# Kernel tuning notes

Hardware: AMD Instinct MI355X
Metric: run time of the kernel (lower is better)

Reference implementation:

```python
import jax, jax.numpy as jnp
import numpy as np

MEAN_DEG = 3.8
QS = (2, 4, 8, 16, 32, 64)
POOL_DIM = 100
BP_ITERS = 10


def _bn(x, g, b):
    # BatchNorm1d in training mode: biased batch statistics over the node dim
    m = x.mean(0)
    v = ((x - m) ** 2).mean(0)
    return g * (x - m) * jax.lax.rsqrt(v + 1e-5) + b


def _gcn_sparse(x, src, dst, n, w, b):
    # GCNConv: add self loops, symmetric deg^-1/2 normalization, scatter-add aggregation
    loop = jnp.arange(n, dtype=src.dtype)
    s2 = jnp.concatenate([src, loop])
    d2 = jnp.concatenate([dst, loop])
    deg = jax.ops.segment_sum(jnp.ones(s2.shape[0], x.dtype), d2, num_segments=n)
    dinv = jnp.where(deg > 0, jax.lax.rsqrt(deg), 0.0)
    norm = (dinv[s2] * dinv[d2])[:, None]
    return jax.ops.segment_sum((x @ w)[s2] * norm, d2, num_segments=n) + b


def _gcn_dense(x, adj, w, b):
    # GCN on the dense pooled adjacency (pooled graphs are fully connected)
    n = adj.shape[-1]
    A = adj + jnp.eye(n, dtype=adj.dtype)
    d = A.sum(-1)
    dinv = jnp.where(d > 0, jax.lax.rsqrt(d), 0.0)
    An = dinv[:, :, None] * A * dinv[:, None, :]
    return jnp.einsum('bij,bjd->bid', An, x @ w) + b


def _bp(src, dst, n, q, beta, seed):
    # SBM-style belief propagation: iterate node marginals psi [n,q] for a fixed
    # number of sweeps; coupling exp(beta), global external field ~ mean_degree.
    key = jax.random.fold_in(jax.random.key(42), seed)
    psi0 = jax.nn.softmax(jax.random.normal(key, (n, q), jnp.float32), -1)
    eb = jnp.expm1(beta)

    def step(psi, _):
        msg = jax.ops.segment_sum(jnp.log1p(eb * psi[src]), dst, num_segments=n)
        field = (MEAN_DEG * beta / n) * psi.sum(0)
        return jax.nn.softmax(msg - field, -1), None

    psi, _ = jax.lax.scan(step, psi0, None, length=BP_ITERS)
    return psi


def _forward(x, w11, b11, g11, be11, w12, b12, g12, be12, w13, b13, g13, be13,
             bp_betas, pool_w, pool_b,
             w21, b21, g21, be21, w22, b22, g22, be22, w23, b23, g23, be23,
             fc1_w, fc1_b, fc2_w, fc2_b, edge_index, num_graphs):
    n = x.shape[0]
    B = num_graphs
    N = n // B
    src, dst = edge_index[0], edge_index[1]
    # per-graph dense adjacency (edge_index_to_csr -> todense, duplicates sum)
    adj = jnp.zeros((B, N, N), x.dtype).at[src // N, src % N, dst % N].add(1.0)

    # stage 1: three GCN + BN layers on the raw graph
    x11 = _bn(_gcn_sparse(x, src, dst, n, w11, b11), g11, be11)
    x12 = _bn(_gcn_sparse(x11, src, dst, n, w12, b12), g12, be12)
    x13 = _bn(_gcn_sparse(x12, src, dst, n, w13, b13), g13, be13)
    x1_out = jnp.concatenate([x11, x12, x13], -1).reshape(B, N, -1).max(1)  # [B,90]

    # six belief-propagation runs -> concat assignments [n, 2+4+...+64 = 126]
    s1 = jnp.concatenate([_bp(src, dst, n, q, bp_betas[i], i) for i, q in enumerate(QS)], -1)
    s1 = s1 @ pool_w + pool_b  # [n, 100]

    # dense diff-pool
    s1 = jax.nn.softmax(s1.reshape(B, N, POOL_DIM), -1)
    p1_x = jnp.einsum('bnk,bnd->bkd', s1, x13.reshape(B, N, -1))   # [B,100,30]
    p1_adj = jnp.einsum('bnk,bnm,bml->bkl', s1, adj, s1)           # [B,100,100]

    # stage 2: three dense GCN + BN layers on pooled graphs
    C = 30
    x21 = _bn(_gcn_dense(p1_x, p1_adj, w21, b21).reshape(-1, C), g21, be21)
    x22 = _bn(_gcn_dense(x21.reshape(B, POOL_DIM, C), p1_adj, w22, b22).reshape(-1, C), g22, be22)
    x23 = _bn(_gcn_dense(x22.reshape(B, POOL_DIM, C), p1_adj, w23, b23).reshape(-1, C), g23, be23)
    x2_out = jnp.concatenate([x21, x22, x23], -1).reshape(B, POOL_DIM, -1).max(1)  # [B,90]

    conv_out = jnp.concatenate([x1_out, x2_out], -1)  # [B,180]
    out = jax.nn.relu(conv_out @ fc1_w + fc1_b) @ fc2_w + fc2_b  # dropout p=0 -> identity
    return out, jnp.zeros((1,), x.dtype)


def setup_inputs() -> dict:
    key = jax.random.key(0)
    B, N, EP = 64, 1024, 8192
    ks = jax.random.split(key, 24)
    x = jax.random.normal(ks[0], (B * N, 3), jnp.float32)
    off = (jnp.arange(B, dtype=jnp.int32) * N)[:, None]
    src = (jax.random.randint(ks[1], (B, EP), 0, N, jnp.int32) + off).reshape(-1)
    dst = (jax.random.randint(ks[2], (B, EP), 0, N, jnp.int32) + off).reshape(-1)
    edge_index = jnp.stack([src, dst])

    def lin(k, i, o):
        return jax.random.normal(k, (i, o), jnp.float32) / np.sqrt(i)

    p = {}
    dims1 = [(3, 30), (30, 30), (30, 30)]
    for idx, (i, o) in enumerate(dims1, 1):
        p['w1%d' % idx] = lin(ks[2 + idx], i, o)
        p['b1%d' % idx] = jnp.zeros((o,), jnp.float32)
        p['g1%d' % idx] = jnp.ones((o,), jnp.float32)
        p['be1%d' % idx] = jnp.zeros((o,), jnp.float32)
    for idx in (1, 2, 3):
        p['w2%d' % idx] = lin(ks[8 + idx], 30, 30)
        p['b2%d' % idx] = jnp.zeros((30,), jnp.float32)
        p['g2%d' % idx] = jnp.ones((30,), jnp.float32)
        p['be2%d' % idx] = jnp.zeros((30,), jnp.float32)
    qs = np.array(QS, np.float32)
    p['bp_betas'] = jnp.asarray(np.log(qs / (np.sqrt(MEAN_DEG) - 1.0) + 1.0))
    p['pool_w'] = lin(ks[15], 126, 100); p['pool_b'] = jnp.zeros((100,), jnp.float32)
    p['fc1_w'] = lin(ks[16], 180, 50); p['fc1_b'] = jnp.zeros((50,), jnp.float32)
    p['fc2_w'] = lin(ks[17], 50, 6); p['fc2_b'] = jnp.zeros((6,), jnp.float32)
    return {'x': x, 'edge_index': edge_index, 'num_graphs': B, **p}


def reference(x, edge_index, num_graphs, w11, b11, g11, be11, w12, b12, g12, be12,
              w13, b13, g13, be13, bp_betas, pool_w, pool_b,
              w21, b21, g21, be21, w22, b22, g22, be22, w23, b23, g23, be23,
              fc1_w, fc1_b, fc2_w, fc2_b):
    return _forward(x, w11, b11, g11, be11, w12, b12, g12, be12, w13, b13, g13, be13,
                    bp_betas, pool_w, pool_b,
                    w21, b21, g21, be21, w22, b22, g22, be22, w23, b23, g23, be23,
                    fc1_w, fc1_b, fc2_w, fc2_b, edge_index, num_graphs)
```

## Files before the change

### kernel.cpp

```cpp
#include <hip/hip_runtime.h>
#include <stdint.h>
#include <float.h>


constexpr int NN    = 65536;
constexpr int NEDGE = 524288;
constexpr int NBG   = 64;

__constant__ int cQS[6]   = {2,4,8,16,32,64};

__device__ __forceinline__ void tf2x32(uint32_t k0, uint32_t k1, uint32_t x0, uint32_t x1,
                                       uint32_t& o0, uint32_t& o1){
  uint32_t ks[3] = {k0, k1, k0 ^ k1 ^ 0x1BD11BDAu};
  x0 += ks[0]; x1 += ks[1];
  const int RA[4] = {13,15,26,6}, RB[4] = {17,29,16,24};
  #pragma unroll
  for (int i=0;i<5;i++){
    const int* r = (i&1)? RB : RA;
    #pragma unroll
    for (int j=0;j<4;j++){
      x0 += x1;
      x1 = (x1 << r[j]) | (x1 >> (32 - r[j]));
      x1 ^= x0;
    }
// ... 199 lines not shown

template<int TPR>
__device__ __forceinline__ void bfly_max4(float& m0, float& m1, float& m2, float& m3){
  if constexpr (TPR > 1){
    #pragma unroll
    for (int lm = TPR>>1; lm; lm >>= 1){
      float p0=__shfl_xor(m0,lm,64), p1=__shfl_xor(m1,lm,64);
      float p2=__shfl_xor(m2,lm,64), p3=__shfl_xor(m3,lm,64);
      m0=fmaxf(m0,p0); m1=fmaxf(m1,p1); m2=fmaxf(m2,p2); m3=fmaxf(m3,p3);
    }
  }
  { float t0=fmaxf(m0,m2), t1=fmaxf(m1,m3), t2=fmaxf(m2,m0), t3=fmaxf(m3,m1);
    m0=t0; m1=t1; m2=t2; m3=t3; }
  { float t0=fmaxf(m0,m1), t1=fmaxf(m1,m0), t2=fmaxf(m2,m3), t3=fmaxf(m3,m2);
    m0=t0; m1=t1; m2=t2; m3=t3; }
}

template<int TPR>
__device__ __forceinline__ void bfly_sum4(float& s0, float& s1, float& s2, float& s3){
  if constexpr (TPR > 1){
    #pragma unroll
    for (int lm = TPR>>1; lm; lm >>= 1){
      float p0=__shfl_xor(s0,lm,64), p1=__shfl_xor(s1,lm,64);
      float p2=__shfl_xor(s2,lm,64), p3=__shfl_xor(s3,lm,64);
      s0 += p0; s1 += p1; s2 += p2; s3 += p3;
    }
  }
  { float t0=s0+s2, t1=s1+s3, t2=s2+s0, t3=s3+s1;
    s0=t0; s1=t1; s2=t2; s3=t3; }
  { float t0=s0+s1, t1=s1+s0, t2=s2+s3, t3=s3+s2;
    s0=t0; s1=t1; s2=t2; s3=t3; }
}

template<int Q, int CO, int TPR, int L2T>
__device__ __forceinline__ void bp_first_elem2(int graph, int jj, float* __restrict__ psi_pk,
                                               float* __restrict__ lg, float eb,
                                               uint32_t k0, uint32_t k1){
  int idx = jj*256 + (int)threadIdx.x;
  if constexpr (Q == 2){
    int row = graph*1024 + idx;
    float z[2];
    #pragma unroll
    for (int r=0;r<2;r++){
      uint32_t b0,b1;
      tf2x32(k0,k1, 0u, (uint32_t)(row*2 + r), b0,b1);
      uint32_t bits = b0 ^ b1;
      float f = __uint_as_float((bits>>9) | 0x3F800000u) - 1.0f;
      const float lo = __uint_as_float(0xBF7FFFFFu);
      float u = fmaxf(lo, f*2.0f + lo);
      z[r] = __uint_as_float(0x3FB504F3u) * erfinv32(u);
    }
    float m0=fmaxf(z[0],z[1]), m1=fmaxf(z[1],z[0]);
    float e0=expf(z[0]-m0), e1=expf(z[1]-m1);
    float s0=e0+e1, s1=e1+e0;
    float p0=e0/s0, p1=e1/s1;
    ((float2*)(psi_pk + (size_t)NN*CO))[row] = make_float2(p0,p1);
    ((float2*)(lg     + (size_t)NN*CO))[row] = make_float2(log1pf(eb*p0), log1pf(eb*p1));
  } else {
    int rw = idx >> L2T, ct = idx & (TPR-1);
    int row = graph*1024 + rw;
    float z[4];
    #pragma unroll
    for (int r=0;r<4;r++){
      uint32_t b0,b1;
      tf2x32(k0,k1, 0u, (uint32_t)(row*Q + 4*ct + r), b0,b1);
      uint32_t bits = b0 ^ b1;
      float f = __uint_as_float((bits>>9) | 0x3F800000u) - 1.0f;
      const float lo = __uint_as_float(0xBF7FFFFFu);
      float u = fmaxf(lo, f*2.0f + lo);
      z[r] = __uint_as_float(0x3FB504F3u) * erfinv32(u);
    }
    float m0=z[0],m1=z[1],m2=z[2],m3=z[3];
    bfly_max4<TPR>(m0,m1,m2,m3);
    float e0=expf(z[0]-m0), e1=expf(z[1]-m1), e2=expf(z[2]-m2), e3=expf(z[3]-m3);
    float s0=e0,s1=e1,s2=e2,s3=e3;
    bfly_sum4<TPR>(s0,s1,s2,s3);
    float p0=e0/s0, p1=e1/s1, p2=e2/s2, p3=e3/s3;
    ((float4*)(psi_pk + (size_t)NN*CO))[(size_t)row*TPR + ct] = make_float4(p0,p1,p2,p3);
    ((float4*)(lg     + (size_t)NN*CO))[(size_t)row*TPR + ct] =
        make_float4(log1pf(eb*p0), log1pf(eb*p1), log1pf(eb*p2), log1pf(eb*p3));
  }
}

__global__ __launch_bounds__(256) void k_bp_first(float* __restrict__ psi_pk, float* __restrict__ lg,
                                                  const float* __restrict__ betas,
                                                  const float* __restrict__ xin,
                                                  const float* __restrict__ w11,
                                                  float* __restrict__ hbuf){
  if (blockIdx.x >= 8192){
    __shared__ float ws[90];
    int t = threadIdx.x;
    for (int i=t;i<90;i+=256) ws[i] = w11[i];
    __syncthreads();
    int id = ((int)blockIdx.x - 8192)*256 + t;
    if (id >= NN*30) return;
    int v = id/30, j = id - v*30;
    const float* xr = xin + v*3;
    float acc = 0.f;
    #pragma unroll
    for (int k=0;k<3;k++) acc += xr[k]*ws[k*30+j];
    hbuf[id] = acc;
    return;
  }
  int graph, run, jj;
  bp_decode2(blockIdx.x, graph, run, jj);
  uint32_t k0, k1;
  tf2x32(0u, 42u, 0u, (uint32_t)run, k0, k1);
  float eb = expm1f(betas[run]);
  switch(run){
    case 0: bp_first_elem2< 2, 0, 1,0>(graph, jj, psi_pk, lg, eb, k0, k1); break;
    case 1: bp_first_elem2< 4, 2, 1,0>(graph, jj, psi_pk, lg, eb, k0, k1); break;
    case 2: bp_first_elem2< 8, 6, 2,1>(graph, jj, psi_pk, lg, eb, k0, k1); break;
    case 3: bp_first_elem2<16,14, 4,2>(graph, jj, psi_pk, lg, eb, k0, k1); break;
    case 4: bp_first_elem2<32,30, 8,3>(graph, jj, psi_pk, lg, eb, k0, k1); break;
    default:bp_first_elem2<64,62,16,4>(graph, jj, psi_pk, lg, eb, k0, k1); break;
  }
}

template<int Q, int CO, int TPR, int L2T>
__device__ __forceinline__ void bp_step_elem2(int graph, int run, int jj,
    const float* __restrict__ lcur, float* __restrict__ nxt, float* __restrict__ lnxt,
    const int* __restrict__ rp, const int* __restrict__ col,
    const float* __restrict__ field, float eb, int fin){
  int idx = jj*256 + (int)threadIdx.x;
  if constexpr (Q == 2){
    int row = graph*1024 + idx;
    const float2* B2 = (const float2*)(lcur + (size_t)NN*CO);
    float a0=0.f, a1=0.f;
    int a = rp[row], b2 = rp[row+1];
    for (; a+8<=b2; a+=8){
      int s0=col[a],s1=col[a+1],s2=col[a+2],s3=col[a+3];
      int s4=col[a+4],s5=col[a+5],s6=col[a+6],s7=col[a+7];
      float2 u0=B2[s0], u1=B2[s1], u2=B2[s2], u3=B2[s3];
      float2 u4=B2[s4], u5=B2[s5], u6=B2[s6], u7=B2[s7];
      a0+=u0.x; a1+=u0.y; a0+=u1.x; a1+=u1.y;
      a0+=u2.x; a1+=u2.y; a0+=u3.x; a1+=u3.y;
      a0+=u4.x; a1+=u4.y; a0+=u5.x; a1+=u5.y;
      a0+=u6.x; a1+=u6.y; a0+=u7.x; a1+=u7.y;
    }
    for (; a+4<=b2; a+=4){
      int s0=col[a],s1=col[a+1],s2=col[a+2],s3=col[a+3];
      float2 u0=B2[s0], u1=B2[s1], u2=B2[s2], u3=B2[s3];
      a0+=u0.x; a1+=u0.y; a0+=u1.x; a1+=u1.y;
      a0+=u2.x; a1+=u2.y; a0+=u3.x; a1+=u3.y;
    }
    for (; a<b2; ++a){ float2 u=B2[col[a]]; a0+=u.x; a1+=u.y; }
    float v0 = a0 - field[run*64 + 0];
    float v1 = a1 - field[run*64 + 1];
    float m0=fmaxf(v0,v1), m1=fmaxf(v1,v0);
    float e0=expf(v0-m0), e1=expf(v1-m1);
    float s0=e0+e1, s1=e1+e0;
    float p0=e0/s0, p1=e1/s1;
    if (fin){
      float* o = nxt + (size_t)row*126 + CO;
      o[0]=p0; o[1]=p1;
    } else {
      ((float2*)(nxt  + (size_t)NN*CO))[row] = make_float2(p0,p1);
      ((float2*)(lnxt + (size_t)NN*CO))[row] = make_float2(log1pf(eb*p0), log1pf(eb*p1));
    }
  } else {
    int rw = idx >> L2T, ct = idx & (TPR-1);
    int row = graph*1024 + rw;
    const float4* B4 = (const float4*)(lcur + (size_t)NN*CO);
    float a0=0.f,a1=0.f,a2=0.f,a3=0.f;
    int a = rp[row], b2 = rp[row+1];
    for (; a+8<=b2; a+=8){
      int s0=col[a],s1=col[a+1],s2=col[a+2],s3=col[a+3];
      int s4=col[a+4],s5=col[a+5],s6=col[a+6],s7=col[a+7];
      float4 u0=B4[(size_t)s0*TPR+ct], u1=B4[(size_t)s1*TPR+ct];
      float4 u2=B4[(size_t)s2*TPR+ct], u3=B4[(size_t)s3*TPR+ct];
      float4 u4=B4[(size_t)s4*TPR+ct], u5=B4[(size_t)s5*TPR+ct];
      float4 u6=B4[(size_t)s6*TPR+ct], u7=B4[(size_t)s7*TPR+ct];
      a0+=u0.x; a1+=u0.y; a2+=u0.z; a3+=u0.w;
      a0+=u1.x; a1+=u1.y; a2+=u1.z; a3+=u1.w;
      a0+=u2.x; a1+=u2.y; a2+=u2.z; a3+=u2.w;
      a0+=u3.x; a1+=u3.y; a2+=u3.z; a3+=u3.w;
      a0+=u4.x; a1+=u4.y; a2+=u4.z; a3+=u4.w;
      a0+=u5.x; a1+=u5.y; a2+=u5.z; a3+=u5.w;
      a0+=u6.x; a1+=u6.y; a2+=u6.z; a3+=u6.w;
      a0+=u7.x; a1+=u7.y; a2+=u7.z; a3+=u7.w;
    }
    for (; a+4<=b2; a+=4){
      int s0=col[a],s1=col[a+1],s2=col[a+2],s3=col[a+3];
      float4 u0=B4[(size_t)s0*TPR+ct], u1=B4[(size_t)s1*TPR+ct];
      float4 u2=B4[(size_t)s2*TPR+ct], u3=B4[(size_t)s3*TPR+ct];
      a0+=u0.x; a1+=u0.y; a2+=u0.z; a3+=u0.w;
      a0+=u1.x; a1+=u1.y; a2+=u1.z; a3+=u1.w;
      a0+=u2.x; a1+=u2.y; a2+=u2.z; a3+=u2.w;
      a0+=u3.x; a1+=u3.y; a2+=u3.z; a3+=u3.w;
    }
    for (; a<b2; ++a){
      float4 u = B4[(size_t)col[a]*TPR+ct];
      a0+=u.x; a1+=u.y; a2+=u.z; a3+=u.w;
    }
    const float4 fld = *(const float4*)(field + run*64 + 4*ct);
    float v0 = a0 - fld.x, v1 = a1 - fld.y, v2 = a2 - fld.z, v3 = a3 - fld.w;
    float m0=v0,m1=v1,m2=v2,m3=v3;
    bfly_max4<TPR>(m0,m1,m2,m3);
    float e0=expf(v0-m0), e1=expf(v1-m1), e2=expf(v2-m2), e3=expf(v3-m3);
    float s0=e0,s1=e1,s2=e2,s3=e3;
    bfly_sum4<TPR>(s0,s1,s2,s3);
    float p0=e0/s0, p1=e1/s1, p2=e2/s2, p3=e3/s3;
    if (fin){
      float* o = nxt + (size_t)row*126 + CO + 4*ct;
      o[0]=p0; o[1]=p1; o[2]=p2; o[3]=p3;
    } else {
      ((float4*)(nxt  + (size_t)NN*CO))[(size_t)row*TPR+ct] = make_float4(p0,p1,p2,p3);
      ((float4*)(lnxt + (size_t)NN*CO))[(size_t)row*TPR+ct] =
          make_float4(log1pf(eb*p0), log1pf(eb*p1), log1pf(eb*p2), log1pf(eb*p3));
    }
  }
}

__global__ __launch_bounds__(256) void k_bp_step(
    float* __restrict__ nxt, const float* __restrict__ lcur, float* __restrict__ lnxt,
    const int* __restrict__ rp, const int* __restrict__ col,
    const float* __restrict__ field, const float* __restrict__ betas, int fin,
    int auxType, const float* __restrict__ aA, const float* __restrict__ aB,
    const float* __restrict__ aC, float* __restrict__ aO,
    float* __restrict__ agS, float* __restrict__ agQ,
    const float* __restrict__ adinv, const float* __restrict__ asfc,
    float* __restrict__ aconv){
  if (blockIdx.x >= 8192){
    __shared__ float smem[960];
    int ab = (int)blockIdx.x - 8192;
    int t = threadIdx.x;
    if (auxType == 1){
      float* binS = smem; float* binQ = smem + 32;
      if (t < 30){ binS[t]=0.f; binQ[t]=0.f; }
      __syncthreads();
      int xcd = ab & 7, i = ab >> 3;
      int gs = i/60, j = i - gs*60;
      int graph = gs*8 + xcd;
      int idwg = j*256 + t;
      int rw = idwg/15, pr = idwg - rw*15;
      int v = graph*1024 + rw;
      float dv = adinv[v];
      float accx = 0.f, accy = 0.f;
      int a = rp[v], e = rp[v+1];
      for (; a+4<=e; a+=4){
        int s0=col[a], s1=col[a+1], s2=col[a+2], s3=col[a+3];
        float d0=adinv[s0], d1=adinv[s1], d2=adinv[s2], d3=adinv[s3];
        float2 h0=*(const float2*)(aA+s0*30+2*pr), h1=*(const float2*)(aA+s1*30+2*pr);
        float2 h2=*(const float2*)(aA+s2*30+2*pr), h3=*(const float2*)(aA+s3*30+2*pr);
        accx += h0.x*(d0*dv); accy += h0.y*(d0*dv);
        accx += h1.x*(d1*dv); accy += h1.y*(d1*dv);
        accx += h2.x*(d2*dv); accy += h2.y*(d2*dv);
        accx += h3.x*(d3*dv); accy += h3.y*(d3*dv);
      }
      for (; a<e; ++a){
        int s = col[a];
        float w = adinv[s]*dv;
        float2 hv = *(const float2*)(aA+s*30+2*pr);
        accx += hv.x*w; accy += hv.y*w;
      }
      float2 hs = *(const float2*)(aA + v*30 + 2*pr);
      float w2 = dv*dv;
      accx += hs.x*w2; accy += hs.y*w2;
      float2 o; o.x = accx + aB[2*pr]; o.y = accy + aB[2*pr+1];
      *(float2*)(aO + v*30 + 2*pr) = o;
      atomicAdd(&binS[2*pr],   o.x); atomicAdd(&binQ[2*pr],   o.x*o.x);
      atomicAdd(&binS[2*pr+1], o.y); atomicAdd(&binQ[2*pr+1], o.y*o.y);
      __syncthreads();
      if (t < 30){
        int slot = (ab & 63)*30 + t;
        atomicAdd(&agS[slot], binS[t]);
        atomicAdd(&agQ[slot], binQ[t]);
      }
    } else if (auxType == 2){
      float* ws = smem; float* cl = smem + 904;
      for (int i=t;i<900;i+=256) ws[i] = aB[i];
      if (t < 30) cl[t] = aC[t];
      __syncthreads();
      int id = ab*256 + t;
      if (id < NN*30){
        int v = id/30, j = id - v*30;
        const float* xr = aA + v*30;
        float acc = cl[j];
        #pragma unroll
        for (int k=0;k<30;k++) acc += xr[k]*ws[k*30+j];
        aO[id] = acc;
      }
    } else if (auxType == 3){
      int b2 = ab & 63, a = ab >> 6;
      const float* X = (a==0)? aA : ((a==1)? aB : aC);
      const float* sf = asfc + a*64;
      float acc[30];
      #pragma unroll
      for (int f=0;f<30;f++) acc[f] = -FLT_MAX;
      for (int r=t; r<1024; r+=256){
        const float* xr = X + (size_t)(b2*1024 + r)*30;
        #pragma unroll
        for (int f=0;f<30;f++) acc[f] = fmaxf(acc[f], sf[f]*xr[f] + sf[32+f]);
      }
      #pragma unroll
      for (int off=32; off; off>>=1){
        #pragma unroll
        for (int f=0;f<30;f++) acc[f] = fmaxf(acc[f], __shfl_xor(acc[f], off, 64));
      }
      int w = t>>6, lane = t&63;
      if (lane == 0){
        #pragma unroll
        for (int f=0;f<30;f++) smem[w*30+f] = acc[f];
      }
      __syncthreads();
      if (t < 30)
        aconv[b2*180 + a*30 + t] =
          fmaxf(fmaxf(smem[t], smem[30+t]), fmaxf(smem[60+t], smem[90+t]));
    }
    return;
  }
  int graph, run, jj;
  bp_decode2(blockIdx.x, graph, run, jj);
  float eb = expm1f(betas[run]);
  switch(run){
    case 0: bp_step_elem2< 2, 0, 1,0>(graph, run, jj, lcur, nxt, lnxt, rp, col, field, eb, fin); break;
    case 1: bp_step_elem2< 4, 2, 1,0>(graph, run, jj, lcur, nxt, lnxt, rp, col, field, eb, fin); break;
    case 2: bp_step_elem2< 8, 6, 2,1>(graph, run, jj, lcur, nxt, lnxt, rp, col, field, eb, fin); break;
    case 3: bp_step_elem2<16,14, 4,2>(graph, run, jj, lcur, nxt, lnxt, rp, col, field, eb, fin); break;
    case 4: bp_step_elem2<32,30, 8,3>(graph, run, jj, lcur, nxt, lnxt, rp, col, field, eb, fin); break;
    default:bp_step_elem2<64,62,16,4>(graph, run, jj, lcur, nxt, lnxt, rp, col, field, eb, fin); break;
  }
}

__global__ __launch_bounds__(64) void k_colsum_part(const float* __restrict__ psi_pk, float* __restrict__ part){
  int b = blockIdx.x;
  int xcd = b & 7, i = b >> 3;
  int gs = i/24, rem = i - gs*24;
  int run = rem >> 2, cg = rem & 3;
  int graph = gs*8 + xcd;
  int chunk = graph*4 + cg;
  int q = cQS[run];
  int co = (run==0)?0:(run==1)?2:(run==2)?6:(run==3)?14:(run==4)?30:62;
  int c = threadIdx.x;
  if (q >= 4){
    int nq = q >> 2;
    if (c >= nq) return;
    const float4* p4 = (const float4*)(psi_pk + (size_t)NN*co + (size_t)chunk*256*q) + c;
    float s0=0.f,s1=0.f,s2=0.f,s3=0.f;
    #pragma unroll 8
    for (int r=0;r<256;r++){
      float4 u = p4[(size_t)r*nq];
      s0+=u.x; s1+=u.y; s2+=u.z; s3+=u.w;
    }
    float* o = part + (run*256 + chunk)*64 + 4*c;
    o[0]=s0; o[1]=s1; o[2]=s2; o[3]=s3;
  } else {
    if (c >= q) return;
    float s = 0.f;
    const float* p = psi_pk + (size_t)NN*co + (size_t)chunk*256*q + c;
    #pragma unroll 8
    for (int r=0;r<256;r++) s += p[r*q];
    part[(run*256 + chunk)*64 + c] = s;
  }
}

__global__ void k_field(const float* __restrict__ part, const float* __restrict__ betas,
                        float* __restrict__ field,
                        int auxFold, float* __restrict__ gS, float* __restrict__ gQ, float n,
                        const float* __restrict__ g, const float* __restrict__ be,
                        const float* __restrict__ wnext, float* __restrict__ sfc,
                        float* __restrict__ wfold, float* __restrict__ cvec){
  if (blockIdx.x == 1){
    if (auxFold < 0) return;
    __shared__ float s_l[30], c_l[30];
    int t = threadIdx.x;
    if (t < 30){
      float s=0.f, q=0.f;
      for (int u=0;u<64;u++){ s += gS[u*30+t]; q += gQ[u*30+t]; }
      float m = s/n;
      float var = q/n - m*m;
      float sc = g[t]*(1.0f/sqrtf(var+1e-5f));
      float c0 = be[t] - sc*m;
      s_l[t]=sc; c_l[t]=c0;
      sfc[t]=sc; sfc[32+t]=c0;
      for (int u=0;u<64;u++){ gS[u*30+t]=0.f; gQ[u*30+t]=0.f; }
    }
    __syncthreads();
    if (auxFold == 1){
      for (int i=t;i<900;i+=384) wfold[i] = s_l[i/30]*wnext[i];
      if (t<30){
        float c=0.f;
        for (int k=0;k<30;k++) c += c_l[k]*wnext[k*30+t];
        cvec[t]=c;
      }
    }
    return;
  }
  int id = threadIdx.x;
  int run = id >> 6, c = id & 63;
  if (c >= cQS[run]) return;
  float s = 0.f;
  for (int b=0;b<256;b++) s += part[(run*256 + b)*64 + c];
  float beta = betas[run];
  field[id] = s * (3.8f*beta/65536.0f);
}

__global__ __launch_bounds__(256) void k_catT(const float* __restrict__ cat, float* __restrict__ catT){
  __shared__ float tile[64*127];
  int b = blockIdx.x, t = threadIdx.x;
  const float* src = cat + (size_t)b*64*126;
  for (int i=t;i<8064;i+=256){
    int r = i/126, k = i - r*126;
    tile[r*127 + k] = src[i];
  }
  __syncthreads();
  for (int i=t;i<8064;i+=256){
    int k = i>>6, r = i&63;
    catT[(size_t)k*65536 + b*64 + r] = tile[r*127 + k];
  }
}

__global__ __launch_bounds__(256) void k_s1t(const float* __restrict__ catT, const float* __restrict__ pw,
                                             const float* __restrict__ pb, float* __restrict__ s1){
  __shared__ float wl[12600];
  __shared__ float pbl[100];
  __shared__ float redM[2][128];
  __shared__ float redS[2][128];
  int t = threadIdx.x;
  for (int i=t;i<12600;i+=256) wl[i] = pw[i];
  if (t < 100) pbl[t] = pb[t];
  int w = t>>6, lane = t&63;
  int rh = w&1, chh = w>>1;
  int ch = chh*50;
  int row = blockIdx.x*128 + rh*64 + lane;
  __syncthreads();
  float acc[50];
  #pragma unroll
  for (int j=0;j<50;j++) acc[j] = pbl[ch+j];
  for (int k=0;k<126;k++){
    float xv = catT[(size_t)k*65536 + row];
    const float* wr = &wl[k*100 + ch];
    #pragma unroll
    for (int j=0;j<50;j+=2){
      float2 wv = *(const float2*)&wr[j];
      acc[j]   += xv*wv.x;
      acc[j+1] += xv*wv.y;
    }
  }
  float m = acc[0];
  #pragma unroll
  for (int j=1;j<50;j++) m = fmaxf(m, acc[j]);
  redM[chh][rh*64 + lane] = m;
  __syncthreads();
  float mm = fmaxf(redM[0][rh*64 + lane], redM[1][rh*64 + lane]);
  float s = 0.f;
  #pragma unroll
  for (int j=0;j<50;j++){ acc[j] = expf(acc[j]-mm); s += acc[j]; }
  redS[chh][rh*64 + lane] = s;
  __syncthreads();
  float tot = redS[0][rh*64 + lane] + redS[1][rh*64 + lane];
  float* o = s1 + (size_t)row*100 + ch;
  #pragma unroll
  for (int j=0;j<50;j+=2){
    float2 ov; ov.x = acc[j]/tot; ov.y = acc[j+1]/tot;
    *(float2*)&o[j] = ov;
  }
}

__global__ __launch_bounds__(256) void k_T(const float* __restrict__ s1, const int* __restrict__ rp,
                                           const int* __restrict__ col, float* __restrict__ T){
  int b = blockIdx.x;
  int xcd = b & 7, i = b >> 3;
  int gs = i/100, j = i - gs*100;
  int graph = gs*8 + xcd;
  int idwg = j*256 + threadIdx.x;
  int rw = idwg/25, quad = idwg - rw*25;
  int v = graph*1024 + rw;
  float a0=0.f,a1=0.f,a2=0.f,a3=0.f;
  const float4* S4 = (const float4*)s1;
  int a = rp[v], e = rp[v+1];
  for (; a+8<=e; a+=8){
    int s0=col[a], s1_=col[a+1], s2=col[a+2], s3=col[a+3];
    int s4=col[a+4], s5=col[a+5], s6=col[a+6], s7=col[a+7];
    float4 u0=S4[(size_t)s0*25+quad], u1=S4[(size_t)s1_*25+quad];
    float4 u2=S4[(size_t)s2*25+quad], u3=S4[(size_t)s3*25+quad];
    float4 u4=S4[(size_t)s4*25+quad], u5=S4[(size_t)s5*25+quad];
    float4 u6=S4[(size_t)s6*25+quad], u7=S4[(size_t)s7*25+quad];
    a0+=u0.x; a1+=u0.y; a2+=u0.z; a3+=u0.w;
    a0+=u1.x; a1+=u1.y; a2+=u1.z; a3+=u1.w;
    a0+=u2.x; a1+=u2.y; a2+=u2.z; a3+=u2.w;
    a0+=u3.x; a1+=u3.y; a2+=u3.z; a3+=u3.w;
    a0+=u4.x; a1+=u4.y; a2+=u4.z; a3+=u4.w;
    a0+=u5.x; a1+=u5.y; a2+=u5.z; a3+=u5.w;
    a0+=u6.x; a1+=u6.y; a2+=u6.z; a3+=u6.w;
    a0+=u7.x; a1+=u7.y; a2+=u7.z; a3+=u7.w;
  }
  for (; a+4<=e; a+=4){
    int s0=col[a], s1_=col[a+1], s2=col[a+2], s3=col[a+3];
    float4 u0=S4[(size_t)s0*25+quad], u1=S4[(size_t)s1_*25+quad];
    float4 u2=S4[(size_t)s2*25+quad], u3=S4[(size_t)s3*25+quad];
    a0+=u0.x; a1+=u0.y; a2+=u0.z; a3+=u0.w;
    a0+=u1.x; a1+=u1.y; a2+=u1.z; a3+=u1.w;
    a0+=u2.x; a1+=u2.y; a2+=u2.z; a3+=u2.w;
    a0+=u3.x; a1+=u3.y; a2+=u3.z; a3+=u3.w;
  }
  for (; a<e; ++a){
    float4 u = S4[(size_t)col[a]*25+quad];
    a0+=u.x; a1+=u.y; a2+=u.z; a3+=u.w;
  }
  ((float4*)T)[(size_t)v*25 + quad] = make_float4(a0,a1,a2,a3);
}

__global__ __launch_bounds__(512) void k_p1ax(const float* __restrict__ s1, const float* __restrict__ T,
                                              const float* __restrict__ y3, const float* __restrict__ sfc,
                                              float* __restrict__ partA, float* __restrict__ partX){
  __shared__ float sS[6400];
  __shared__ float sT[6400];
  int t = threadIdx.x;
  if (blockIdx.x < 256){
    int blk = blockIdx.x;
    int b = blk >> 2, qtr = blk & 3;
    int tk = t/20, tl = t - tk*20;
    bool act = t < 500;
    int k0 = tk*4, l0 = tl*5;
    float acc[4][5];
    #pragma unroll
    for (int i=0;i<4;i++)
      #pragma unroll
      for (int j=0;j<5;j++) acc[i][j] = 0.f;
    const float* s1b = s1 + (size_t)b*102400;
    const float* Tb  = T  + (size_t)b*102400;
    for (int c=qtr*4; c<qtr*4+4; c++){
      for (int i=t;i<6400;i+=512){ sS[i] = s1b[c*6400+i]; sT[i] = Tb[c*6400+i]; }
      __syncthreads();
      if (act){
        #pragma unroll 2
        for (int n=0;n<64;n++){
          const float* sr = &sS[n*100 + k0];
          const float* tr = &sT[n*100 + l0];
          float s0=sr[0], s1v=sr[1], s2=sr[2], s3=sr[3];
          float t0=tr[0], t1=tr[1], t2=tr[2], t3=tr[3], t4=tr[4];
          acc[0][0]+=s0*t0; acc[0][1]+=s0*t1; acc[0][2]+=s0*t2; acc[0][3]+=s0*t3; acc[0][4]+=s0*t4;
          acc[1][0]+=s1v*t0; acc[1][1]+=s1v*t1; acc[1][2]+=s1v*t2; acc[1][3]+=s1v*t3; acc[1][4]+=s1v*t4;
          acc[2][0]+=s2*t0; acc[2][1]+=s2*t1; acc[2][2]+=s2*t2; acc[2][3]+=s2*t3; acc[2][4]+=s2*t4;
          acc[3][0]+=s3*t0; acc[3][1]+=s3*t1; acc[3][2]+=s3*t2; acc[3][3]+=s3*t3; acc[3][4]+=s3*t4;
        }
      }
      __syncthreads();
    }
    if (act){
      float* pp = partA + (size_t)qtr*640000 + (size_t)b*10000;
      #pragma unroll
      for (int i=0;i<4;i++){
        float* o = pp + (k0+i)*100 + l0;
        #pragma unroll
        for (int j=0;j<5;j++) o[j] = acc[i][j];
      }
    }
  } else {
    int blk = blockIdx.x - 256;
    int b = blk >> 2, qtr = blk & 3;
    float* sX = sT;
    int tk = t/10, tl = t - tk*10;
    bool act = t < 250;
    int k0 = tk*4, d0 = tl*3;
    float acc[4][3];
    #pragma unroll
    for (int i=0;i<4;i++)
      #pragma unroll
      for (int j=0;j<3;j++) acc[i][j] = 0.f;
    const float* s1b = s1 + (size_t)b*102400;
    const float* xb  = y3 + (size_t)b*30720;
// ... 71 lines not shown
  int t = threadIdx.x;
  if (t < 30){ binS[t]=0.f; binQ[t]=0.f; }
  __syncthreads();
  int id = blockIdx.x*256 + t;
  if (id < NBG*100*30){
    int d = id % 30;
    int bk = id / 30;
    int b = bk / 100;
    const float* Ar = An + bk*100;
    const float* hb = h + b*100*30;
    float acc = 0.f;
    for (int l=0;l<100;l++) acc += Ar[l]*hb[l*30+d];
    float val = acc + bias[d];
    y[id] = val;
    atomicAdd(&binS[d], val);
    atomicAdd(&binQ[d], val*val);
  }
  __syncthreads();
  if (t < 30){
    int slot = (blockIdx.x & 63)*30 + t;
    atomicAdd(&gS[slot], binS[t]);
    atomicAdd(&gQ[slot], binQ[t]);
  }
}

__global__ __launch_bounds__(256) void k_pool2(const float* __restrict__ A,
    const float* __restrict__ Bv, const float* __restrict__ Cv,
    const float* __restrict__ sfcBase,
    int rows, float* __restrict__ conv, int coff){
  __shared__ float lds[256*31];
  int b = blockIdx.x, a = blockIdx.y, t = threadIdx.x;
  const float* X = (a==0)? A : ((a==1)? Bv : Cv);
  const float* sf = sfcBase + a*64;
  float acc[30];
  #pragma unroll
  for (int f=0;f<30;f++) acc[f] = -FLT_MAX;
  for (int r=t; r<rows; r+=256){
    const float* xr = X + (size_t)(b*rows + r)*30;
    #pragma unroll
    for (int f=0;f<30;f++) acc[f] = fmaxf(acc[f], sf[f]*xr[f] + sf[32+f]);
  }
  #pragma unroll
  for (int f=0;f<30;f++) lds[t*31+f] = acc[f];
  __syncthreads();
  for (int s=128;s>0;s>>=1){
    if (t<s){
      #pragma unroll
      for (int f=0;f<30;f++) lds[t*31+f] = fmaxf(lds[t*31+f], lds[(t+s)*31+f]);
    }
    __syncthreads();
  }
  if (t<30) conv[b*180 + coff + a*30 + t] = lds[t];
}

__global__ __launch_bounds__(64) void k_fc(const float* __restrict__ conv,
    const float* __restrict__ w1, const float* __restrict__ b1,
    const float* __restrict__ w2, const float* __restrict__ b2, float* __restrict__ out){
  __shared__ float row[180];
  __shared__ float hid[50];
  int b = blockIdx.x, t = threadIdx.x;
  for (int i=t;i<180;i+=64) row[i] = conv[b*180+i];
  __syncthreads();
  if (t < 50){
    float a = b1[t];
    for (int i=0;i<180;i++) a += row[i]*w1[i*50+t];
    hid[t] = fmaxf(a, 0.f);
  }
  __syncthreads();
  if (t < 6){
    float a = b2[t];
    for (int i=0;i<50;i++) a += hid[i]*w2[i*6+t];
    out[b*6+t] = a;
  }
  if (b==0 && t==63) out[NBG*6] = 0.0f;
}

extern "C" void kernel_launch(void* const* d_in, const int* in_sizes, int n_in,
                              void* d_out, int out_size, void* d_ws, size_t ws_size,
                              hipStream_t stream)
{
  (void)in_sizes; (void)n_in; (void)out_size; (void)ws_size;
  const float* x   = (const float*)d_in[0];
  const int*   src = (const int*)d_in[1];
  const int*   dst = src + NEDGE;
  const float* w11=(const float*)d_in[3],  *b11=(const float*)d_in[4],  *g11=(const float*)d_in[5],  *be11=(const float*)d_in[6];
  const float* w12=(const float*)d_in[7],  *b12=(const float*)d_in[8],  *g12=(const float*)d_in[9],  *be12=(const float*)d_in[10];
  const float* w13=(const float*)d_in[11], *b13=(const float*)d_in[12], *g13=(const float*)d_in[13], *be13=(const float*)d_in[14];
  const float* w21=(const float*)d_in[15], *b21=(const float*)d_in[16], *g21=(const float*)d_in[17], *be21=(const float*)d_in[18];
  const float* w22=(const float*)d_in[19], *b22=(const float*)d_in[20], *g22=(const float*)d_in[21], *be22=(const float*)d_in[22];
  const float* w23=(const float*)d_in[23], *b23=(const float*)d_in[24], *g23=(const float*)d_in[25], *be23=(const float*)d_in[26];
  const float* betas=(const float*)d_in[27];
  const float* poolw=(const float*)d_in[28], *poolb=(const float*)d_in[29];
  const float* fc1w=(const float*)d_in[30], *fc1b=(const float*)d_in[31];
  const float* fc2w=(const float*)d_in[32], *fc2b=(const float*)d_in[33];
  float* out = (float*)d_out;

  uint8_t* basep = (uint8_t*)d_ws;
  size_t off = 0;
  auto take = [&](size_t bytes)->void*{
    void* p = basep + off;
    off = (off + bytes + 255) & ~(size_t)255;
    return p;
  };
  int* degi    = (int*)take((size_t)NN*4);
  int* dego    = (int*)take((size_t)NN*4);
  int* cntA    = (int*)take((size_t)NN*4);
  int* cntB    = (int*)take((size_t)NN*4);
  float* gS    = (float*)take(64*30*4);
  float* gQ    = (float*)take(64*30*4);
  int* rp_in   = (int*)take((size_t)(NN+1)*4);
  int* rp_out  = (int*)take((size_t)(NN+1)*4);
  int* bsum    = (int*)take(512*4);
  int* col_in  = (int*)take((size_t)NEDGE*4);
  int* col_out = (int*)take((size_t)NEDGE*4);
  float* dinv  = (float*)take((size_t)NN*4);
  float* hbuf  = (float*)take((size_t)NN*30*4);
  float* X1    = (float*)take((size_t)NN*30*4);
  float* X2    = (float*)take((size_t)NN*30*4);
  float* X3    = (float*)take((size_t)NN*30*4);
  float* bufA  = (float*)take((size_t)NN*126*4);
  float* bufB  = (float*)take((size_t)NN*126*4);
  float* logA  = (float*)take((size_t)NN*126*4);
  float* logB  = (float*)take((size_t)NN*126*4);
  float* partCS= (float*)take((size_t)6*256*64*4);
  float* fieldv= (float*)take(384*4);
  float* sfcAll= (float*)take(6*64*4);
  float* wfold = (float*)take(960*4);
  float* cvec  = (float*)take(32*4);
  float* px    = (float*)take(192000*4);
  float* An    = (float*)take(640000*4);
  float* h2    = (float*)take(192000*4);
  float* X21   = (float*)take(192000*4);
  float* X22   = (float*)take(192000*4);
  float* X23   = (float*)take(192000*4);
  float* conv  = (float*)take(64*180*4);

  float* catT     = logA;
  float* pAdjPart = logB;
  float* pPxPart  = logB + 2560000;

  hipMemsetAsync(degi, 0, (size_t)4*NN*4 + 2*64*30*4, stream);
  k_count<<<2048,256,0,stream>>>(src,dst,degi,dego);
  k_scan1<<<dim3(256,2),256,0,stream>>>(degi, dego, rp_in, rp_out, bsum);
  k_scan2<<<2,256,0,stream>>>(bsum);
  k_scan3<<<dim3(256,2),256,0,stream>>>(rp_in, rp_out, bsum);
  k_fill<<<dim3(2048,2),256,0,stream>>>(src, dst, rp_in, rp_out, cntA, cntB, col_in, col_out);
  k_sortrow<<<dim3(256,2),256,0,stream>>>(rp_in, rp_out, col_in, col_out, src, dst, degi, dinv);

  k_bp_first<<<15872,256,0,stream>>>(bufA, logA, betas, x, w11, hbuf);

  float* cur = bufA;  float* nxt = bufB;
  float* lcur = logA; float* lnxt = logB;
  for (int it=0; it<10; ++it){
    k_colsum_part<<<1536,64,0,stream>>>(cur, partCS);
    int fold = (it==1||it==3)? 1 : ((it==5)? 0 : -1);
    const float* gg = (it==1)? g11 : ((it==3)? g12 : g13);
    const float* bb = (it==1)? be11: ((it==3)? be12: be13);
    const float* wn = (it==1)? w12 : ((it==3)? w13 : nullptr);
    float* sfc = (it==1)? sfcAll : ((it==3)? sfcAll+64 : sfcAll+128);
    k_field<<<2,384,0,stream>>>(partCS, betas, fieldv, fold, gS, gQ, 65536.f,
                                gg, bb, wn, sfc, wfold, cvec);
    int fin = (it==9);
    int auxType = 0, auxN = 0;
    const float *aA=nullptr, *aB=nullptr, *aC=nullptr; float *aO=nullptr;
    if      (it==0){ auxType=1; auxN=3840; aA=hbuf; aB=b11; aO=X1; }
    else if (it==1){ auxType=2; auxN=7680; aA=X1; aB=wfold; aC=cvec; aO=hbuf; }
    else if (it==2){ auxType=1; auxN=3840; aA=hbuf; aB=b12; aO=X2; }
    else if (it==3){ auxType=2; auxN=7680; aA=X2; aB=wfold; aC=cvec; aO=hbuf; }
    else if (it==4){ auxType=1; auxN=3840; aA=hbuf; aB=b13; aO=X3; }
    else if (it==5){ auxType=3; auxN=192;  aA=X1; aB=X2; aC=X3; }
    k_bp_step<<<8192+auxN,256,0,stream>>>(nxt, lcur, lnxt, rp_in, col_in, fieldv, betas, fin,
        auxType, aA, aB, aC, aO, gS, gQ, dinv, sfcAll, conv);
    float* tp = cur;  cur = nxt;   nxt = tp;
    float* tl = lcur; lcur = lnxt; lnxt = tl;
  }

  k_catT<<<1024,256,0,stream>>>(bufA, catT);
  k_s1t<<<512,256,0,stream>>>(catT, poolw, poolb, bufB);
  k_T<<<6400,256,0,stream>>>(bufB, rp_out, col_out, bufA);
  k_p1ax<<<512,512,0,stream>>>(bufB, bufA, X3, sfcAll+128, pAdjPart, pPxPart);
  k_anpx<<<814,256,0,stream>>>(pAdjPart, pPxPart, An, px);

  k_mm30<30><<<750,256,0,stream>>>(px, w21, h2, NBG*100);
  k_y2<<<750,256,0,stream>>>(An, h2, b21, X21, gS, gQ);
  k_bnw<1><<<1,256,0,stream>>>(gS, gQ, 6400.f, g21, be21, w22, sfcAll+3*64, wfold, cvec);
  k_mm30c<<<750,256,0,stream>>>(X21, wfold, cvec, h2, NBG*100);
  k_y2<<<750,256,0,stream>>>(An, h2, b22, X22, gS, gQ);
  k_bnw<1><<<1,256,0,stream>>>(gS, gQ, 6400.f, g22, be22, w23, sfcAll+4*64, wfold, cvec);
  k_mm30c<<<750,256,0,stream>>>(X22, wfold, cvec, h2, NBG*100);
  k_y2<<<750,256,0,stream>>>(An, h2, b23, X23, gS, gQ);
  k_bnw<0><<<1,256,0,stream>>>(gS, gQ, 6400.f, g23, be23, nullptr, sfcAll+5*64, nullptr, nullptr);
  k_pool2<<<dim3(NBG,3),256,0,stream>>>(X21, X22, X23, sfcAll+3*64, 100, conv, 90);

  k_fc<<<64,64,0,stream>>>(conv, fc1w, fc1b, fc2w, fc2b, out);
}
```

Baseline: 1.235 ms.

## Move aux GCN work into colsum kernel and write final BP output transposed

Aux GCN/BN/pool blocks are moved from the BP step kernel into a widened colsum kernel that packs four colsum groups per 256-thread block, and the BN fold schedule is shifted one iteration earlier to match. The last BP step writes probabilities directly in feature-major layout, removing the separate transpose kernel. This drops a launch and a full pass over the concatenated marginals. In exchange, the aux work no longer overlaps with the BP sweep, and the final-step stores become strided.

```diff
diff --git a/kernel.cpp b/kernel.cpp
--- a/kernel.cpp
+++ b/kernel.cpp
@@ -375,8 +375,8 @@
     float s0=e0+e1, s1=e1+e0;
     float p0=e0/s0, p1=e1/s1;
     if (fin){
-      float* o = nxt + (size_t)row*126 + CO;
-      o[0]=p0; o[1]=p1;
+      nxt[(size_t)(CO+0)*NN + row] = p0;
+      nxt[(size_t)(CO+1)*NN + row] = p1;
     } else {
       ((float2*)(nxt  + (size_t)NN*CO))[row] = make_float2(p0,p1);
       ((float2*)(lnxt + (size_t)NN*CO))[row] = make_float2(log1pf(eb*p0), log1pf(eb*p1));
@@ -425,8 +425,11 @@
     bfly_sum4<TPR>(s0,s1,s2,s3);
     float p0=e0/s0, p1=e1/s1, p2=e2/s2, p3=e3/s3;
     if (fin){
-      float* o = nxt + (size_t)row*126 + CO + 4*ct;
-      o[0]=p0; o[1]=p1; o[2]=p2; o[3]=p3;
+      int kb = CO + 4*ct;
+      nxt[(size_t)(kb+0)*NN + row] = p0;
+      nxt[(size_t)(kb+1)*NN + row] = p1;
+      nxt[(size_t)(kb+2)*NN + row] = p2;
+      nxt[(size_t)(kb+3)*NN + row] = p3;
     } else {
       ((float4*)(nxt  + (size_t)NN*CO))[(size_t)row*TPR+ct] = make_float4(p0,p1,p2,p3);
       ((float4*)(lnxt + (size_t)NN*CO))[(size_t)row*TPR+ct] =
@@ -438,101 +441,7 @@
 __global__ __launch_bounds__(256) void k_bp_step(
     float* __restrict__ nxt, const float* __restrict__ lcur, float* __restrict__ lnxt,
     const int* __restrict__ rp, const int* __restrict__ col,
-    const float* __restrict__ field, const float* __restrict__ betas, int fin,
-    int auxType, const float* __restrict__ aA, const float* __restrict__ aB,
-    const float* __restrict__ aC, float* __restrict__ aO,
-    float* __restrict__ agS, float* __restrict__ agQ,
-    const float* __restrict__ adinv, const float* __restrict__ asfc,
-    float* __restrict__ aconv){
-  if (blockIdx.x >= 8192){
-    __shared__ float smem[960];
-    int ab = (int)blockIdx.x - 8192;
-    int t = threadIdx.x;
-    if (auxType == 1){
-      float* binS = smem; float* binQ = smem + 32;
-      if (t < 30){ binS[t]=0.f; binQ[t]=0.f; }
-      __syncthreads();
-      int xcd = ab & 7, i = ab >> 3;
-      int gs = i/60, j = i - gs*60;
-      int graph = gs*8 + xcd;
-      int idwg = j*256 + t;
-      int rw = idwg/15, pr = idwg - rw*15;
-      int v = graph*1024 + rw;
-      float dv = adinv[v];
-      float accx = 0.f, accy = 0.f;
-      int a = rp[v], e = rp[v+1];
-      for (; a+4<=e; a+=4){
-        int s0=col[a], s1=col[a+1], s2=col[a+2], s3=col[a+3];
-        float d0=adinv[s0], d1=adinv[s1], d2=adinv[s2], d3=adinv[s3];
-        float2 h0=*(const float2*)(aA+s0*30+2*pr), h1=*(const float2*)(aA+s1*30+2*pr);
-        float2 h2=*(const float2*)(aA+s2*30+2*pr), h3=*(const float2*)(aA+s3*30+2*pr);
-        accx += h0.x*(d0*dv); accy += h0.y*(d0*dv);
-        accx += h1.x*(d1*dv); accy += h1.y*(d1*dv);
-        accx += h2.x*(d2*dv); accy += h2.y*(d2*dv);
-        accx += h3.x*(d3*dv); accy += h3.y*(d3*dv);
-      }
-      for (; a<e; ++a){
-        int s = col[a];
-        float w = adinv[s]*dv;
-        float2 hv = *(const float2*)(aA+s*30+2*pr);
-        accx += hv.x*w; accy += hv.y*w;
-      }
-      float2 hs = *(const float2*)(aA + v*30 + 2*pr);
-      float w2 = dv*dv;
-      accx += hs.x*w2; accy += hs.y*w2;
-      float2 o; o.x = accx + aB[2*pr]; o.y = accy + aB[2*pr+1];
-      *(float2*)(aO + v*30 + 2*pr) = o;
-      atomicAdd(&binS[2*pr],   o.x); atomicAdd(&binQ[2*pr],   o.x*o.x);
-      atomicAdd(&binS[2*pr+1], o.y); atomicAdd(&binQ[2*pr+1], o.y*o.y);
-      __syncthreads();
-      if (t < 30){
-        int slot = (ab & 63)*30 + t;
-        atomicAdd(&agS[slot], binS[t]);
-        atomicAdd(&agQ[slot], binQ[t]);
-      }
-    } else if (auxType == 2){
-      float* ws = smem; float* cl = smem + 904;
-      for (int i=t;i<900;i+=256) ws[i] = aB[i];
-      if (t < 30) cl[t] = aC[t];
-      __syncthreads();
-      int id = ab*256 + t;
-      if (id < NN*30){
-        int v = id/30, j = id - v*30;
-        const float* xr = aA + v*30;
-        float acc = cl[j];
-        #pragma unroll
-        for (int k=0;k<30;k++) acc += xr[k]*ws[k*30+j];
-        aO[id] = acc;
-      }
-    } else if (auxType == 3){
-      int b2 = ab & 63, a = ab >> 6;
-      const float* X = (a==0)? aA : ((a==1)? aB : aC);
-      const float* sf = asfc + a*64;
-      float acc[30];
-      #pragma unroll
-      for (int f=0;f<30;f++) acc[f] = -FLT_MAX;
-      for (int r=t; r<1024; r+=256){
-        const float* xr = X + (size_t)(b2*1024 + r)*30;
-        #pragma unroll
-        for (int f=0;f<30;f++) acc[f] = fmaxf(acc[f], sf[f]*xr[f] + sf[32+f]);
-      }
-      #pragma unroll
-      for (int off=32; off; off>>=1){
-        #pragma unroll
-        for (int f=0;f<30;f++) acc[f] = fmaxf(acc[f], __shfl_xor(acc[f], off, 64));
-      }
-      int w = t>>6, lane = t&63;
-      if (lane == 0){
-        #pragma unroll
-        for (int f=0;f<30;f++) smem[w*30+f] = acc[f];
-      }
-      __syncthreads();
-      if (t < 30)
-        aconv[b2*180 + a*30 + t] =
-          fmaxf(fmaxf(smem[t], smem[30+t]), fmaxf(smem[60+t], smem[90+t]));
-    }
-    return;
-  }
+    const float* __restrict__ field, const float* __restrict__ betas, int fin){
   int graph, run, jj;
   bp_decode2(blockIdx.x, graph, run, jj);
   float eb = expm1f(betas[run]);
@@ -546,35 +455,130 @@
   }
 }
 
-__global__ __launch_bounds__(64) void k_colsum_part(const float* __restrict__ psi_pk, float* __restrict__ part){
-  int b = blockIdx.x;
-  int xcd = b & 7, i = b >> 3;
-  int gs = i/24, rem = i - gs*24;
-  int run = rem >> 2, cg = rem & 3;
-  int graph = gs*8 + xcd;
-  int chunk = graph*4 + cg;
-  int q = cQS[run];
-  int co = (run==0)?0:(run==1)?2:(run==2)?6:(run==3)?14:(run==4)?30:62;
-  int c = threadIdx.x;
-  if (q >= 4){
-    int nq = q >> 2;
-    if (c >= nq) return;
-    const float4* p4 = (const float4*)(psi_pk + (size_t)NN*co + (size_t)chunk*256*q) + c;
-    float s0=0.f,s1=0.f,s2=0.f,s3=0.f;
-    #pragma unroll 8
-    for (int r=0;r<256;r++){
-      float4 u = p4[(size_t)r*nq];
-      s0+=u.x; s1+=u.y; s2+=u.z; s3+=u.w;
-    }
-    float* o = part + (run*256 + chunk)*64 + 4*c;
-    o[0]=s0; o[1]=s1; o[2]=s2; o[3]=s3;
-  } else {
-    if (c >= q) return;
-    float s = 0.f;
-    const float* p = psi_pk + (size_t)NN*co + (size_t)chunk*256*q + c;
-    #pragma unroll 8
-    for (int r=0;r<256;r++) s += p[r*q];
-    part[(run*256 + chunk)*64 + c] = s;
+__global__ __launch_bounds__(256) void k_colsum(const float* __restrict__ psi_pk,
+    float* __restrict__ part, const int* __restrict__ rp, const int* __restrict__ col,
+    int auxType, const float* __restrict__ aA, const float* __restrict__ aB,
+    const float* __restrict__ aC, float* __restrict__ aO,
+    float* __restrict__ agS, float* __restrict__ agQ,
+    const float* __restrict__ adinv, const float* __restrict__ asfc,
+    float* __restrict__ aconv){
+  __shared__ float smem[960];
+  int t = threadIdx.x;
+  if (blockIdx.x < 384){
+    int grp = t >> 6, c = t & 63;
+    int b = blockIdx.x*4 + grp;
+    int xcd = b & 7, i = b >> 3;
+    int gs = i/24, rem = i - gs*24;
+    int run = rem >> 2, cg = rem & 3;
+    int graph = gs*8 + xcd;
+    int chunk = graph*4 + cg;
+    int q = cQS[run];
+    int co = (run==0)?0:(run==1)?2:(run==2)?6:(run==3)?14:(run==4)?30:62;
+    if (q >= 4){
+      int nq = q >> 2;
+      if (c >= nq) return;
+      const float4* p4 = (const float4*)(psi_pk + (size_t)NN*co + (size_t)chunk*256*q) + c;
+      float s0=0.f,s1=0.f,s2=0.f,s3=0.f;
+      #pragma unroll 8
+      for (int r=0;r<256;r++){
+        float4 u = p4[(size_t)r*nq];
+        s0+=u.x; s1+=u.y; s2+=u.z; s3+=u.w;
+      }
+      float* o = part + (run*256 + chunk)*64 + 4*c;
+      o[0]=s0; o[1]=s1; o[2]=s2; o[3]=s3;
+    } else {
+      if (c >= q) return;
+      float s = 0.f;
+      const float* p = psi_pk + (size_t)NN*co + (size_t)chunk*256*q + c;
+      #pragma unroll 8
+      for (int r=0;r<256;r++) s += p[r*q];
+      part[(run*256 + chunk)*64 + c] = s;
+    }
+    return;
+  }
+  int ab = (int)blockIdx.x - 384;
+  if (auxType == 1){
+    float* binS = smem; float* binQ = smem + 32;
+    if (t < 30){ binS[t]=0.f; binQ[t]=0.f; }
+    __syncthreads();
+    int xcd = ab & 7, i = ab >> 3;
+    int gs = i/60, j = i - gs*60;
+    int graph = gs*8 + xcd;
+    int idwg = j*256 + t;
+    int rw = idwg/15, pr = idwg - rw*15;
+    int v = graph*1024 + rw;
+    float dv = adinv[v];
+    float accx = 0.f, accy = 0.f;
+    int a = rp[v], e = rp[v+1];
+    for (; a+4<=e; a+=4){
+      int s0=col[a], s1=col[a+1], s2=col[a+2], s3=col[a+3];
+      float d0=adinv[s0], d1=adinv[s1], d2=adinv[s2], d3=adinv[s3];
+      float2 h0=*(const float2*)(aA+s0*30+2*pr), h1=*(const float2*)(aA+s1*30+2*pr);
+      float2 h2=*(const float2*)(aA+s2*30+2*pr), h3=*(const float2*)(aA+s3*30+2*pr);
+      accx += h0.x*(d0*dv); accy += h0.y*(d0*dv);
+      accx += h1.x*(d1*dv); accy += h1.y*(d1*dv);
+      accx += h2.x*(d2*dv); accy += h2.y*(d2*dv);
+      accx += h3.x*(d3*dv); accy += h3.y*(d3*dv);
+    }
+    for (; a<e; ++a){
+      int s = col[a];
+      float w = adinv[s]*dv;
+      float2 hv = *(const float2*)(aA+s*30+2*pr);
+      accx += hv.x*w; accy += hv.y*w;
+    }
+    float2 hs = *(const float2*)(aA + v*30 + 2*pr);
+    float w2 = dv*dv;
+    accx += hs.x*w2; accy += hs.y*w2;
+    float2 o; o.x = accx + aB[2*pr]; o.y = accy + aB[2*pr+1];
+    *(float2*)(aO + v*30 + 2*pr) = o;
+    atomicAdd(&binS[2*pr],   o.x); atomicAdd(&binQ[2*pr],   o.x*o.x);
+    atomicAdd(&binS[2*pr+1], o.y); atomicAdd(&binQ[2*pr+1], o.y*o.y);
+    __syncthreads();
+    if (t < 30){
+      int slot = (ab & 63)*30 + t;
+      atomicAdd(&agS[slot], binS[t]);
+      atomicAdd(&agQ[slot], binQ[t]);
+    }
+  } else if (auxType == 2){
+    float* ws = smem; float* cl = smem + 904;
+    for (int i=t;i<900;i+=256) ws[i] = aB[i];
+    if (t < 30) cl[t] = aC[t];
+    __syncthreads();
+    int id = ab*256 + t;
+    if (id < NN*30){
+      int v = id/30, j = id - v*30;
+      const float* xr = aA + v*30;
+      float acc = cl[j];
+      #pragma unroll
+      for (int k=0;k<30;k++) acc += xr[k]*ws[k*30+j];
+      aO[id] = acc;
+    }
+  } else if (auxType == 3){
+    int b2 = ab & 63, a = ab >> 6;
+    const float* X = (a==0)? aA : ((a==1)? aB : aC);
+    const float* sf = asfc + a*64;
+    float acc[30];
+    #pragma unroll
+    for (int f=0;f<30;f++) acc[f] = -FLT_MAX;
+    for (int r=t; r<1024; r+=256){
+      const float* xr = X + (size_t)(b2*1024 + r)*30;
+      #pragma unroll
+      for (int f=0;f<30;f++) acc[f] = fmaxf(acc[f], sf[f]*xr[f] + sf[32+f]);
+    }
+    #pragma unroll
+    for (int off=32; off; off>>=1){
+      #pragma unroll
+      for (int f=0;f<30;f++) acc[f] = fmaxf(acc[f], __shfl_xor(acc[f], off, 64));
+    }
+    int w = t>>6, lane = t&63;
+    if (lane == 0){
+      #pragma unroll
+      for (int f=0;f<30;f++) smem[w*30+f] = acc[f];
+    }
+    __syncthreads();
+    if (t < 30)
+      aconv[b2*180 + a*30 + t] =
+        fmaxf(fmaxf(smem[t], smem[30+t]), fmaxf(smem[60+t], smem[90+t]));
   }
 }
 
@@ -617,21 +621,6 @@
   for (int b=0;b<256;b++) s += part[(run*256 + b)*64 + c];
   float beta = betas[run];
   field[id] = s * (3.8f*beta/65536.0f);
-}
-
-__global__ __launch_bounds__(256) void k_catT(const float* __restrict__ cat, float* __restrict__ catT){
-  __shared__ float tile[64*127];
-  int b = blockIdx.x, t = threadIdx.x;
-  const float* src = cat + (size_t)b*64*126;
-  for (int i=t;i<8064;i+=256){
-    int r = i/126, k = i - r*126;
-    tile[r*127 + k] = src[i];
-  }
-  __syncthreads();
-  for (int i=t;i<8064;i+=256){
-    int k = i>>6, r = i&63;
-    catT[(size_t)k*65536 + b*64 + r] = tile[r*127 + k];
-  }
 }
 
 __global__ __launch_bounds__(256) void k_s1t(const float* __restrict__ catT, const float* __restrict__ pw,
@@ -1009,15 +998,6 @@
   float* cur = bufA;  float* nxt = bufB;
   float* lcur = logA; float* lnxt = logB;
   for (int it=0; it<10; ++it){
-    k_colsum_part<<<1536,64,0,stream>>>(cur, partCS);
-    int fold = (it==1||it==3)? 1 : ((it==5)? 0 : -1);
-    const float* gg = (it==1)? g11 : ((it==3)? g12 : g13);
-    const float* bb = (it==1)? be11: ((it==3)? be12: be13);
-    const float* wn = (it==1)? w12 : ((it==3)? w13 : nullptr);
-    float* sfc = (it==1)? sfcAll : ((it==3)? sfcAll+64 : sfcAll+128);
-    k_field<<<2,384,0,stream>>>(partCS, betas, fieldv, fold, gS, gQ, 65536.f,
-                                gg, bb, wn, sfc, wfold, cvec);
-    int fin = (it==9);
     int auxType = 0, auxN = 0;
     const float *aA=nullptr, *aB=nullptr, *aC=nullptr; float *aO=nullptr;
     if      (it==0){ auxType=1; auxN=3840; aA=hbuf; aB=b11; aO=X1; }
@@ -1026,13 +1006,22 @@
     else if (it==3){ auxType=2; auxN=7680; aA=X2; aB=wfold; aC=cvec; aO=hbuf; }
     else if (it==4){ auxType=1; auxN=3840; aA=hbuf; aB=b13; aO=X3; }
     else if (it==5){ auxType=3; auxN=192;  aA=X1; aB=X2; aC=X3; }
-    k_bp_step<<<8192+auxN,256,0,stream>>>(nxt, lcur, lnxt, rp_in, col_in, fieldv, betas, fin,
+    k_colsum<<<384+auxN,256,0,stream>>>(cur, partCS, rp_in, col_in,
         auxType, aA, aB, aC, aO, gS, gQ, dinv, sfcAll, conv);
+    int fold = (it==0||it==2)? 1 : ((it==4)? 0 : -1);
+    const float* gg = (it==0)? g11 : ((it==2)? g12 : g13);
+    const float* bb = (it==0)? be11: ((it==2)? be12: be13);
+    const float* wn = (it==0)? w12 : ((it==2)? w13 : nullptr);
+    float* sfc = (it==0)? sfcAll : ((it==2)? sfcAll+64 : sfcAll+128);
+    k_field<<<2,384,0,stream>>>(partCS, betas, fieldv, fold, gS, gQ, 65536.f,
+                                gg, bb, wn, sfc, wfold, cvec);
+    int fin = (it==9);
+    float* stepNxt = fin ? catT : nxt;
+    k_bp_step<<<8192,256,0,stream>>>(stepNxt, lcur, lnxt, rp_in, col_in, fieldv, betas, fin);
     float* tp = cur;  cur = nxt;   nxt = tp;
     float* tl = lcur; lcur = lnxt; lnxt = tl;
   }
 
-  k_catT<<<1024,256,0,stream>>>(bufA, catT);
   k_s1t<<<512,256,0,stream>>>(catT, poolw, poolb, bufB);
   k_T<<<6400,256,0,stream>>>(bufB, rp_out, col_out, bufA);
   k_p1ax<<<512,512,0,stream>>>(bufB, bufA, X3, sfcAll+128, pAdjPart, pPxPart);
```

Result: faster. 1.182 ms (-4.3%).
